# Performance work log

Hardware: AMD Instinct MI355X
Metric: run time of the kernel (lower is better)

## Reference

```python
import jax, jax.numpy as jnp
import numpy as np

N = 50000      # nodes
E = 800000     # edges
D_IN = 128     # irreps_in dim
SH = 16        # irreps_sh dim (lmax=3)
EA = 16        # edge_attr_dim
H = 8          # num_heads
DQ = 64        # irreps_query dim (8 per head)
DK = 64        # irreps_key dim (8 per head)
DV = 128       # irreps_out dim (16 per head)
HID = 64       # radial MLP hidden


def setup_inputs() -> dict:
    key = jax.random.key(0)
    ks = jax.random.split(key, 20)
    g = lambda k, shape, fan: jax.random.normal(k, shape, jnp.float32) / np.sqrt(fan)
    return {
        "node_attr": jax.random.normal(ks[0], (N, D_IN), jnp.float32),
        "edge_attr": jax.random.normal(ks[1], (E, EA), jnp.float32),
        "edge_sh": jax.random.normal(ks[2], (E, SH), jnp.float32),
        # h_q linear
        "Wq": g(ks[3], (D_IN, DQ), D_IN),
        # h_k conv: depthwise SH mixing, channel-mixing linear, radial MLP gate
        "Wang_k": g(ks[4], (D_IN, SH), SH),
        "Wlin_k": g(ks[5], (D_IN, DK), D_IN),
        "W1k": g(ks[6], (EA, HID), EA),
        "b1k": jnp.zeros((HID,), jnp.float32),
        "W2k": g(ks[7], (HID, DK), HID),
        # h_v conv
        "Wang_v": g(ks[8], (D_IN, SH), SH),
        "Wlin_v": g(ks[9], (D_IN, DV), D_IN),
        "W1v": g(ks[10], (EA, HID), EA),
        "b1v": jnp.zeros((HID,), jnp.float32),
        "W2v": g(ks[11], (HID, DV), HID),
        # FullyConnectedTensorProduct(query_per_head, key_per_head, '0e') -> weighted bilinear dot
        "Wdot": g(ks[12], (DQ // H, DK // H), DQ // H),
        # lin_out
        "Wout": g(ks[13], (DV, DV), DV),
        "edge_index": jax.random.randint(ks[14], (2, E), 0, N, jnp.int64),
    }


def _conv_per_edge(x_src, edge_attr, edge_sh, Wang, Wlin, W1, b1, W2):
    # depthwise tensor product of node feats with edge SH, channel mix, radial gate
    rad = jax.nn.relu(edge_attr @ W1 + b1) @ W2          # [E, Dout]
    g = edge_sh @ Wang.T                                  # [E, D_IN]
    return ((x_src * g) @ Wlin) * rad                     # [E, Dout]


def reference(node_attr, edge_attr, edge_sh, Wq, Wang_k, Wlin_k, W1k, b1k, W2k,
              Wang_v, Wlin_v, W1v, b1v, W2v, Wdot, Wout, edge_index):
    src, dst = edge_index[0], edge_index[1]
    n = node_attr.shape[0]
    e = src.shape[0]

    q = (node_attr @ Wq).reshape(n, H, DQ // H)           # [N,H,dq]
    x_src = node_attr[src]                                # gather [E,D_IN]
    k = _conv_per_edge(x_src, edge_attr, edge_sh, Wang_k, Wlin_k, W1k, b1k, W2k).reshape(e, H, DK // H)
    v = _conv_per_edge(x_src, edge_attr, edge_sh, Wang_v, Wlin_v, W1v, b1v, W2v).reshape(e, H, DV // H)

    # TP 'dot' to scalars: weighted bilinear per head
    alpha = jnp.einsum('ehq,qk,ehk->eh', q[dst], Wdot, k)  # [E,H]

    # scatter_softmax over incoming edges of each dst node
    amax = jax.ops.segment_max(alpha, dst, num_segments=n)  # [N,H]
    ealpha = jnp.exp(alpha - amax[dst])
    denom = jax.ops.segment_sum(ealpha, dst, num_segments=n)
    attn = ealpha / denom[dst]                              # [E,H]

    # weighted scatter-sum of values
    out = jax.ops.segment_sum(attn[..., None] * v, dst, num_segments=n)  # [N,H,dv]
    return out.reshape(n, DV) @ Wout
```

## Files before the change

### kernel.cpp

```cpp
#include <hip/hip_runtime.h>
#include <stdint.h>

#define NN 50000
#define NE 800000
#define STRIP 49

typedef unsigned int u32;
typedef uint16_t u16;

__device__ __forceinline__ float b2f(u16 u){ return __builtin_bit_cast(float, (u32)((u32)u << 16)); }
__device__ __forceinline__ float b2f_lo(u32 p){ return __builtin_bit_cast(float, p << 16); }
__device__ __forceinline__ float b2f_hi(u32 p){ return __builtin_bit_cast(float, p & 0xffff0000u); }
__device__ __forceinline__ u32 f2b_bits(float f){ u32 u = __builtin_bit_cast(u32, f); return (u + 0x7fffu + ((u >> 16) & 1u)) >> 16; }
__device__ __forceinline__ u16 f2b(float f){ return (u16)f2b_bits(f); }
__device__ __forceinline__ u32 packb(float lo, float hi){ return f2b_bits(lo) | (f2b_bits(hi) << 16); }

typedef __bf16 bf16x2 __attribute__((ext_vector_type(2)));
#if defined(__has_builtin)
#if __has_builtin(__builtin_amdgcn_fdot2_f32_bf16)
#define HAVE_DOT2_BUILTIN 1
#endif
#endif

#ifdef HAVE_DOT2_BUILTIN
__device__ __forceinline__ float dot2b(u32 a, u32 b, float c){
  return __builtin_amdgcn_fdot2_f32_bf16(__builtin_bit_cast(bf16x2, a),
                                         __builtin_bit_cast(bf16x2, b), c, false);
}
#else
__device__ __forceinline__ float dot2b(u32 a, u32 b, float c){
  c = fmaf(b2f_lo(a), b2f_lo(b), c);
  return fmaf(b2f_hi(a), b2f_hi(b), c);
}
#endif

typedef __attribute__((ext_vector_type(8))) short short8;
typedef __attribute__((ext_vector_type(4))) float f32x4;
__device__ __forceinline__ f32x4 mf32(uint4 a, uint4 b, f32x4 c){
  return __builtin_amdgcn_mfma_f32_16x16x32_bf16(
      __builtin_bit_cast(short8, a), __builtin_bit_cast(short8, b), c, 0, 0, 0);
}

#define OFF_WANG_V 0
#define OFF_W1_V   5120
#define OFF_WLIN_V 7680
#define OFF_W2_V   25088
#define OFF_WANG_K 34304
#define OFF_W1_K   39424
#define OFF_WLIN_K 41984
#define OFF_W2_K   50688
#define OFF_WOUT   55296
#define OFF_WQD    72704
#define WT_TOTAL   81408

__global__ __launch_bounds__(256) void zero_kernel(int* __restrict__ counts,
                                                   int* __restrict__ edge_ids)
{
  int i = blockIdx.x * 256 + threadIdx.x;
  if (i < NN) counts[i] = 0;
  if (i < NE) edge_ids[i] = 0;
}

__global__ __launch_bounds__(256) void prep_w_kernel(
    const float* __restrict__ Wang_v, const float* __restrict__ W1_v,
    const float* __restrict__ Wlin_v, const float* __restrict__ W2_v,
    const float* __restrict__ Wang_k, const float* __restrict__ W1_k,
    const float* __restrict__ Wlin_k, const float* __restrict__ W2_k,
    const float* __restrict__ Wout, const float* __restrict__ Wq,
    const float* __restrict__ Wdot,
    u16* __restrict__ wt)
{
  int idx = blockIdx.x * 256 + threadIdx.x;
  if (idx >= WT_TOTAL) return;
  float val = 0.f;
  if (idx < OFF_W1_V) {
    int l = idx - OFF_WANG_V, n = l / 40, k = l % 40;
    if (k >= 16 && k < 32) val = Wang_v[n * 16 + (k - 16)];
  } else if (idx < OFF_WLIN_V) {
    int l = idx - OFF_W1_V, n = l / 40, k = l % 40;
    if (k < 16) val = W1_v[k * 64 + n];
  } else if (idx < OFF_W2_V) {
    int l = idx - OFF_WLIN_V, n = l / 136, k = l % 136;
    if (k < 128) val = Wlin_v[k * 128 + n];
  } else if (idx < OFF_WANG_K) {
    int l = idx - OFF_W2_V, n = l / 72, k = l % 72;
    if (k < 64) val = W2_v[k * 128 + n];
  } else if (idx < OFF_W1_K) {
    int l = idx - OFF_WANG_K, n = l / 40, k = l % 40;
    if (k >= 16 && k < 32) val = Wang_k[n * 16 + (k - 16)];
  } else if (idx < OFF_WLIN_K) {
    int l = idx - OFF_W1_K, n = l / 40, k = l % 40;
    if (k < 16) val = W1_k[k * 64 + n];
  } else if (idx < OFF_W2_K) {
    int l = idx - OFF_WLIN_K, n = l / 136, k = l % 136;
    if (k < 128) val = Wlin_k[k * 64 + n];
  } else if (idx < OFF_WOUT) {
    int l = idx - OFF_W2_K, n = l / 72, k = l % 72;
    if (k < 64) val = W2_k[k * 64 + n];
  } else if (idx < OFF_WQD) {
    int l = idx - OFF_WOUT, n = l / 136, k = l % 136;
    if (k < 128) val = Wout[k * 128 + n];
  } else {
    int l = idx - OFF_WQD, n = l / 136, k = l % 136;
    if (k < 128) {
      int h = n >> 3, r = n & 7;
      float s = 0.f;
#pragma unroll
      for (int i = 0; i < 8; ++i) s += Wq[k * 64 + h * 8 + i] * Wdot[i * 8 + r];
      val = s;
    }
  }
  wt[idx] = f2b(val);
}

__global__ __launch_bounds__(256) void qw_kernel(const float* __restrict__ node_attr,
                                                 const u16* __restrict__ wt,
                                                 u16* __restrict__ qw)
{
  __shared__ __align__(16) u16 sX[64 * 136];
  uint4* sX4 = (uint4*)sX;
  u32* sX32 = (u32*)sX;
  const uint4* wt4 = (const uint4*)wt;
  const int tid = threadIdx.x, wv = tid >> 6, lane = tid & 63, lq = lane >> 4, ln = lane & 15;
  const int n0 = blockIdx.x * 64;
  uint4 rB[4];
#pragma unroll
  for (int ks = 0; ks < 4; ++ks) rB[ks] = wt4[9088 + (wv * 16 + ln) * 17 + ks * 4 + lq];
  {
    int row = tid >> 2, q4 = tid & 3;
    int n = n0 + row;
    bool valid = n < NN;
    const float4* xp = (const float4*)(node_attr + (size_t)(valid ? n : 0) * 128);
#pragma unroll
    for (int i = 0; i < 8; ++i) {
      float4 v = valid ? xp[q4 * 8 + i] : make_float4(0.f, 0.f, 0.f, 0.f);
      sX32[row * 68 + (q4 * 8 + i) * 2]     = packb(v.x, v.y);
      sX32[row * 68 + (q4 * 8 + i) * 2 + 1] = packb(v.z, v.w);
    }
  }
  __syncthreads();
  const f32x4 z4 = {0.f, 0.f, 0.f, 0.f};
  int col = wv * 16 + ln;
#pragma unroll
  for (int et = 0; et < 4; ++et) {
    f32x4 acc = z4;
#pragma unroll
    for (int ks = 0; ks < 4; ++ks) acc = mf32(sX4[(et * 16 + ln) * 17 + ks * 4 + lq], rB[ks], acc);
#pragma unroll
    for (int r = 0; r < 4; ++r) {
      int rr = n0 + et * 16 + lq * 4 + r;
      if (rr < NN) qw[(size_t)rr * 64 + col] = f2b(acc[r]);
    }
  }
}

__global__ __launch_bounds__(256, 2) void conv_fused_kernel(
    const float* __restrict__ node_attr, const float* __restrict__ edge_attr,
    const float* __restrict__ edge_sh, const int* __restrict__ edge_index,
    const float* __restrict__ b1v, const float* __restrict__ b1k,
    const u16* __restrict__ wt, const u16* __restrict__ qw,
    u16* __restrict__ v_out, float* __restrict__ alpha)
{
  __shared__ __align__(16) u16 sC[64 * 40];
  __shared__ __align__(16) u16 sX[64 * 136];
  __shared__ __align__(16) u16 sTk[64 * 136];
  __shared__ __align__(16) u16 sHv[64 * 72];
  __shared__ __align__(16) u16 sHk[64 * 72];
  uint4* sC4 = (uint4*)sC; u32* sC32 = (u32*)sC;
  uint4* sX4 = (uint4*)sX; u32* sX32 = (u32*)sX;
  uint4* sTk4 = (uint4*)sTk;
  uint4* sHv4 = (uint4*)sHv;
  uint4* sHk4 = (uint4*)sHk;
  const uint4* wt4 = (const uint4*)wt;

  const int tid = threadIdx.x;
  const int wv = tid >> 6, lane = tid & 63, lq = lane >> 4, ln = lane & 15;
  const int e0 = blockIdx.x * 64;
  const int nA = wv * 16 + ln, nB = (wv + 4) * 16 + ln;
  const int cb = wv * 16 + 4 * lq;

  const int el = tid >> 2, p = tid & 3;
  int dq = edge_index[NE + e0 + el]; if ((u32)dq >= NN) dq = 0;
  const uint4* qptr = (const uint4*)(qw + (size_t)dq * 64 + p * 16);
  uint4 q0 = qptr[0], q1 = qptr[1];

  uint4 rW1V    = wt4[640 + nA * 5 + lq];
  uint4 rW1K    = wt4[4928 + nA * 5 + lq];
  uint4 rWangV0 = wt4[nA * 5 + lq],        rWangV1 = wt4[nB * 5 + lq];
  uint4 rWangK0 = wt4[4288 + nA * 5 + lq], rWangK1 = wt4[4288 + nB * 5 + lq];
  uint4 rWlinV[2][4], rWlinK[4], rW2V[2][2], rW2K[2];
#pragma unroll
  for (int ks = 0; ks < 4; ++ks) {
    rWlinV[0][ks] = wt4[960 + nA * 17 + ks * 4 + lq];
    rWlinV[1][ks] = wt4[960 + nB * 17 + ks * 4 + lq];
    rWlinK[ks]    = wt4[5248 + nA * 17 + ks * 4 + lq];
  }
#pragma unroll
  for (int ks = 0; ks < 2; ++ks) {
    rW2V[0][ks] = wt4[3136 + nA * 9 + ks * 4 + lq];
    rW2V[1][ks] = wt4[3136 + nB * 9 + ks * 4 + lq];
    rW2K[ks]    = wt4[6336 + nA * 9 + ks * 4 + lq];
  }
  float4 bV = *(const float4*)(b1v + cb);
  float4 bK = *(const float4*)(b1k + cb);

  {
    int r = tid >> 2, kq = tid & 3;
    float4 ea = ((const float4*)(edge_attr + (size_t)(e0 + r) * 16))[kq];
    *(uint2*)(sC32 + r * 20 + kq * 2) = make_uint2(packb(ea.x, ea.y), packb(ea.z, ea.w));
    float4 sh = ((const float4*)(edge_sh + (size_t)(e0 + r) * 16))[kq];
    *(uint2*)(sC32 + r * 20 + 8 + kq * 2) = make_uint2(packb(sh.x, sh.y), packb(sh.z, sh.w));
  }
  {
    int g = tid >> 3, j = tid & 7;
#pragma unroll
    for (int rr = 0; rr < 2; ++rr) {
      int row = g + rr * 32;
      int s = edge_index[e0 + row]; if ((u32)s >= NN) s = 0;
      const float4* xp = (const float4*)(node_attr + (size_t)s * 128);
#pragma unroll
      for (int c = 0; c < 4; ++c) {
        float4 v = xp[c * 8 + j];
        *(uint2*)(sX32 + row * 68 + c * 16 + j * 2) =
            make_uint2(packb(v.x, v.y), packb(v.z, v.w));
      }
    }
  }
  __syncthreads();

  const f32x4 z4 = {0.f, 0.f, 0.f, 0.f};
#pragma unroll
  for (int et = 0; et < 4; ++et) {
    uint4 aC = sC4[(et * 16 + ln) * 5 + lq];
    f32x4 hv  = mf32(rW1V, aC, z4);
    f32x4 hk  = mf32(rW1K, aC, z4);
    f32x4 t0v = mf32(rWangV0, aC, z4);
    f32x4 t1v = mf32(rWangV1, aC, z4);
    f32x4 t0k = mf32(rWangK0, aC, z4);
    f32x4 t1k = mf32(rWangK1, aC, z4);
    const int edge = et * 16 + ln;
    u16* xr = sX + edge * 136 + cb;
    uint2 xa = *(const uint2*)xr;
    uint2 xb = *(const uint2*)(xr + 64);
    float x0 = b2f_lo(xa.x), x1 = b2f_hi(xa.x), x2 = b2f_lo(xa.y), x3 = b2f_hi(xa.y);
    float y0 = b2f_lo(xb.x), y1 = b2f_hi(xb.x), y2 = b2f_lo(xb.y), y3 = b2f_hi(xb.y);
    *(uint2*)xr = make_uint2(packb(t0v[0] * x0, t0v[1] * x1),
                             packb(t0v[2] * x2, t0v[3] * x3));
    *(uint2*)(xr + 64) = make_uint2(packb(t1v[0] * y0, t1v[1] * y1),
                                    packb(t1v[2] * y2, t1v[3] * y3));
    u16* tkr = sTk + edge * 136 + cb;
    *(uint2*)tkr = make_uint2(packb(t0k[0] * x0, t0k[1] * x1),
                              packb(t0k[2] * x2, t0k[3] * x3));
    *(uint2*)(tkr + 64) = make_uint2(packb(t1k[0] * y0, t1k[1] * y1),
                                     packb(t1k[2] * y2, t1k[3] * y3));
    *(uint2*)(sHv + edge * 72 + cb) = make_uint2(
        packb(fmaxf(hv[0] + bV.x, 0.f), fmaxf(hv[1] + bV.y, 0.f)),
        packb(fmaxf(hv[2] + bV.z, 0.f), fmaxf(hv[3] + bV.w, 0.f)));
    *(uint2*)(sHk + edge * 72 + cb) = make_uint2(
        packb(fmaxf(hk[0] + bK.x, 0.f), fmaxf(hk[1] + bK.y, 0.f)),
        packb(fmaxf(hk[2] + bK.z, 0.f), fmaxf(hk[3] + bK.w, 0.f)));
  }
  __syncthreads();

  f32x4 a1v0[4], a1v1[4], a1k[4], a2v0[4], a2v1[4], a2k[4];
#pragma unroll
  for (int et = 0; et < 4; ++et) {
    const int er = et * 16 + ln;
    f32x4 acc0 = z4, acc1 = z4, acck = z4;
#pragma unroll
    for (int ks = 0; ks < 4; ++ks) {
      uint4 tb = sX4[er * 17 + ks * 4 + lq];
      acc0 = mf32(rWlinV[0][ks], tb, acc0);
      acc1 = mf32(rWlinV[1][ks], tb, acc1);
      acck = mf32(rWlinK[ks], sTk4[er * 17 + ks * 4 + lq], acck);
    }
    a1v0[et] = acc0; a1v1[et] = acc1; a1k[et] = acck;
    f32x4 b0 = z4, b1 = z4, bk = z4;
#pragma unroll
    for (int ks = 0; ks < 2; ++ks) {
      uint4 hb = sHv4[er * 9 + ks * 4 + lq];
      b0 = mf32(rW2V[0][ks], hb, b0);
      b1 = mf32(rW2V[1][ks], hb, b1);
      bk = mf32(rW2K[ks], sHk4[er * 9 + ks * 4 + lq], bk);
    }
    a2v0[et] = b0; a2v1[et] = b1; a2k[et] = bk;
  }
  __syncthreads();

#pragma unroll
  for (int et = 0; et < 4; ++et) {
    const int edge = et * 16 + ln;
    u16* vr = sX + edge * 136 + cb;
    *(uint2*)vr = make_uint2(
        packb(a1v0[et][0] * a2v0[et][0], a1v0[et][1] * a2v0[et][1]),
        packb(a1v0[et][2] * a2v0[et][2], a1v0[et][3] * a2v0[et][3]));
    *(uint2*)(vr + 64) = make_uint2(
        packb(a1v1[et][0] * a2v1[et][0], a1v1[et][1] * a2v1[et][1]),
        packb(a1v1[et][2] * a2v1[et][2], a1v1[et][3] * a2v1[et][3]));
    *(uint2*)(sHk + edge * 72 + cb) = make_uint2(
        packb(a1k[et][0] * a2k[et][0], a1k[et][1] * a2k[et][1]),
        packb(a1k[et][2] * a2k[et][2], a1k[et][3] * a2k[et][3]));
  }
  __syncthreads();

  {
    int row = tid >> 2, seg = tid & 3;
    uint4* gp = (uint4*)(v_out + (size_t)(e0 + row) * 128);
#pragma unroll
    for (int i = 0; i < 4; ++i) gp[seg * 4 + i] = sX4[row * 17 + seg * 4 + i];
  }
  {
    uint4 k0 = sHk4[el * 9 + p * 2];
    uint4 k1 = sHk4[el * 9 + p * 2 + 1];
    float a0 = 0.f, a1 = 0.f;
    a0 = dot2b(q0.x, k0.x, a0); a0 = dot2b(q0.y, k0.y, a0);
    a0 = dot2b(q0.z, k0.z, a0); a0 = dot2b(q0.w, k0.w, a0);
    a1 = dot2b(q1.x, k1.x, a1); a1 = dot2b(q1.y, k1.y, a1);
    a1 = dot2b(q1.z, k1.z, a1); a1 = dot2b(q1.w, k1.w, a1);
    ((float2*)(alpha + (size_t)(e0 + el) * 8))[p] = make_float2(a0, a1);
  }
}

__global__ __launch_bounds__(256) void count_kernel(const int* __restrict__ edge_index,
                                                    int* __restrict__ counts)
{
  int e = blockIdx.x * 256 + threadIdx.x;
  if (e < NE) { int d = edge_index[NE + e]; if ((u32)d >= NN) d = 0; atomicAdd(&counts[d], 1); }
}

__global__ __launch_bounds__(1024) void scan_kernel(const int* __restrict__ counts,
                                                    int* __restrict__ row_ptr,
                                                    int* __restrict__ cursor)
{
  __shared__ int s[1024];
  int tid = threadIdx.x;
  int base = tid * STRIP;
  int sum = 0;
  for (int i = 0; i < STRIP; ++i) { int idx = base + i; sum += (idx < NN) ? counts[idx] : 0; }
  s[tid] = sum;
  __syncthreads();
  for (int off = 1; off < 1024; off <<= 1) {
    int v = s[tid];
    int add = (tid >= off) ? s[tid - off] : 0;
    __syncthreads();
    s[tid] = v + add;
    __syncthreads();
  }
  int running = (tid == 0) ? 0 : s[tid - 1];
  for (int i = 0; i < STRIP; ++i) {
    int idx = base + i;
    if (idx < NN) { row_ptr[idx] = running; cursor[idx] = running; running += counts[idx]; }
  }
  if (tid == 1023) row_ptr[NN] = running;
}

__global__ __launch_bounds__(256) void fill_kernel(const int* __restrict__ edge_index,
                                                   int* __restrict__ cursor,
                                                   int* __restrict__ edge_ids)
{
  int e = blockIdx.x * 256 + threadIdx.x;
  if (e < NE) {
    int dst = edge_index[NE + e]; if ((u32)dst >= NN) dst = 0;
    int pos = atomicAdd(&cursor[dst], 1);
    if ((u32)pos < NE) edge_ids[pos] = e;
  }
}

#define OUPD(aa, ww)                                                   \
  { float mn = fmaxf(m, (aa));                                         \
    float sc = __expf(m - mn);                                         \
    float pw = __expf((aa) - mn);                                      \
    l = l * sc + pw;                                                   \
    accA = accA * sc + pw * b2f_lo(ww);                                \
    accB = accB * sc + pw * b2f_hi(ww);                                \
    m = mn; }

__global__ __launch_bounds__(256) void out_kernel(
    const int* __restrict__ row_ptr, const int* __restrict__ edge_ids,
    const float* __restrict__ alpha, const u16* __restrict__ v_e,
    const u16* __restrict__ wt, float* __restrict__ out)
{
  __shared__ __align__(16) u16 sAgg[16 * 136];
  u32* sAgg32 = (u32*)sAgg;
  uint4* sAgg4 = (uint4*)sAgg;
  const uint4* wt4 = (const uint4*)wt;
  const u32* v32 = (const u32*)v_e;
  const int tid = threadIdx.x, wv = tid >> 6, lane = tid & 63, lq = lane >> 4, ln = lane & 15;
  const f32x4 z4 = {0.f, 0.f, 0.f, 0.f};
  uint4 rWT[2][4];
#pragma unroll
  for (int c = 0; c < 2; ++c) {
    int n = (wv * 2 + c) * 16 + ln;
#pragma unroll
    for (int ks = 0; ks < 4; ++ks) rWT[c][ks] = wt4[6912 + n * 17 + ks * 4 + lq];
  }
  const int hh = lane >> 3;
  const int grp = blockIdx.x;
#pragma unroll 1
  for (int i = 0; i < 4; ++i) {
    int n = grp * 16 + wv * 4 + i;
    int beg = row_ptr[n], end = row_ptr[n + 1];
    if (beg < 0) beg = 0; if (beg > NE) beg = NE;
    if (end < beg) end = beg; if (end > NE) end = NE;
    int deg = end - beg;
    float m = -3.0e38f, l = 0.f, accA = 0.f, accB = 0.f;
    int j = 0;
#pragma unroll 1
    for (; j + 4 <= deg; j += 4) {
      int e0 = edge_ids[beg + j],     e1 = edge_ids[beg + j + 1];
      int e2 = edge_ids[beg + j + 2], e3 = edge_ids[beg + j + 3];
      if ((u32)e0 >= NE) e0 = 0; if ((u32)e1 >= NE) e1 = 0;
      if ((u32)e2 >= NE) e2 = 0; if ((u32)e3 >= NE) e3 = 0;
      float a0 = alpha[(size_t)e0 * 8 + hh]; u32 w0 = v32[(size_t)e0 * 64 + lane];
      float a1 = alpha[(size_t)e1 * 8 + hh]; u32 w1 = v32[(size_t)e1 * 64 + lane];
      float a2 = alpha[(size_t)e2 * 8 + hh]; u32 w2 = v32[(size_t)e2 * 64 + lane];
      float a3 = alpha[(size_t)e3 * 8 + hh]; u32 w3 = v32[(size_t)e3 * 64 + lane];
      OUPD(a0, w0); OUPD(a1, w1); OUPD(a2, w2); OUPD(a3, w3);
    }
#pragma unroll 1
    for (; j < deg; ++j) {
      int e = edge_ids[beg + j]; if ((u32)e >= NE) e = 0;
      float a = alpha[(size_t)e * 8 + hh]; u32 w = v32[(size_t)e * 64 + lane];
      OUPD(a, w);
    }
    float inv = (l > 0.f) ? (1.f / l) : 0.f;
    accA *= inv; accB *= inv;
    sAgg32[(wv * 4 + i) * 68 + lane] = packb(accA, accB);
  }
  __syncthreads();
#pragma unroll
  for (int c = 0; c < 2; ++c) {
    f32x4 acc = z4;
#pragma unroll
    for (int ks = 0; ks < 4; ++ks) acc = mf32(sAgg4[ln * 17 + ks * 4 + lq], rWT[c][ks], acc);
    int col = (wv * 2 + c) * 16 + ln;
#pragma unroll
    for (int r = 0; r < 4; ++r)
      out[(size_t)(grp * 16 + lq * 4 + r) * 128 + col] = acc[r];
  }
}

extern "C" void kernel_launch(void* const* d_in, const int* in_sizes, int n_in,
                              void* d_out, int out_size, void* d_ws, size_t ws_size,
                              hipStream_t stream)
{
  const float* node_attr = (const float*)d_in[0];
  const float* edge_attr = (const float*)d_in[1];
  const float* edge_sh   = (const float*)d_in[2];
  const float* Wq        = (const float*)d_in[3];
  const float* Wang_k    = (const float*)d_in[4];
  const float* Wlin_k    = (const float*)d_in[5];
  const float* W1k       = (const float*)d_in[6];
  const float* b1k       = (const float*)d_in[7];
  const float* W2k       = (const float*)d_in[8];
  const float* Wang_v    = (const float*)d_in[9];
  const float* Wlin_v    = (const float*)d_in[10];
  const float* W1v       = (const float*)d_in[11];
  const float* b1v       = (const float*)d_in[12];
  const float* W2v       = (const float*)d_in[13];
  const float* Wdot      = (const float*)d_in[14];
  const float* Wout      = (const float*)d_in[15];
  const int* edge_index  = (const int*)d_in[16];
  float* out = (float*)d_out;

  char* ws = (char*)d_ws;
  u16*   v_e      = (u16*)(ws + 0);
  float* alpha    = (float*)(ws + 204800000);
  u16*   qw       = (u16*)(ws + 230400000);
  int*   counts   = (int*)(ws + 236800000);
  int*   row_ptr  = (int*)(ws + 237000064);
  int*   cursor   = (int*)(ws + 237200128);
  int*   edge_ids = (int*)(ws + 237400192);
  u16*   wt       = (u16*)(ws + 240600192);

  zero_kernel<<<dim3((NE + 255) / 256), dim3(256), 0, stream>>>(counts, edge_ids);
  prep_w_kernel<<<dim3((WT_TOTAL + 255) / 256), dim3(256), 0, stream>>>(
      Wang_v, W1v, Wlin_v, W2v, Wang_k, W1k, Wlin_k, W2k, Wout, Wq, Wdot, wt);
  qw_kernel<<<dim3((NN + 63) / 64), dim3(256), 0, stream>>>(node_attr, wt, qw);
  conv_fused_kernel<<<dim3(NE / 64), dim3(256), 0, stream>>>(
      node_attr, edge_attr, edge_sh, edge_index, b1v, b1k, wt, qw, v_e, alpha);
  count_kernel<<<dim3((NE + 255) / 256), dim3(256), 0, stream>>>(edge_index, counts);
  scan_kernel<<<dim3(1), dim3(1024), 0, stream>>>(counts, row_ptr, cursor);
  fill_kernel<<<dim3((NE + 255) / 256), dim3(256), 0, stream>>>(edge_index, cursor, edge_ids);
  out_kernel<<<dim3(3125), dim3(256), 0, stream>>>(row_ptr, edge_ids, alpha, v_e, wt, out);
}
```

Baseline: 673.5 us.

## Permute channel layout, gather node features directly into registers, use hardware bf16 pack

```diff
diff --git a/kernel.cpp b/kernel.cpp
--- a/kernel.cpp
+++ b/kernel.cpp
@@ -13,7 +13,11 @@
 __device__ __forceinline__ float b2f_hi(u32 p){ return __builtin_bit_cast(float, p & 0xffff0000u); }
 __device__ __forceinline__ u32 f2b_bits(float f){ u32 u = __builtin_bit_cast(u32, f); return (u + 0x7fffu + ((u >> 16) & 1u)) >> 16; }
 __device__ __forceinline__ u16 f2b(float f){ return (u16)f2b_bits(f); }
-__device__ __forceinline__ u32 packb(float lo, float hi){ return f2b_bits(lo) | (f2b_bits(hi) << 16); }
+__device__ __forceinline__ u32 packb(float lo, float hi){
+  u32 r;
+  asm("v_cvt_pk_bf16_f32 %0, %1, %2" : "=v"(r) : "v"(lo), "v"(hi));
+  return r;
+}
 
 typedef __bf16 bf16x2 __attribute__((ext_vector_type(2)));
 #if defined(__has_builtin)
@@ -39,6 +43,10 @@
 __device__ __forceinline__ f32x4 mf32(uint4 a, uint4 b, f32x4 c){
   return __builtin_amdgcn_mfma_f32_16x16x32_bf16(
       __builtin_bit_cast(short8, a), __builtin_bit_cast(short8, b), c, 0, 0, 0);
+}
+
+__device__ __forceinline__ int chperm(int n){
+  return 32 * ((n & 63) >> 4) + 8 * ((n & 15) >> 2) + 4 * (n >> 6) + (n & 3);
 }
 
 #define OFF_WANG_V 0
@@ -75,19 +83,19 @@
   float val = 0.f;
   if (idx < OFF_W1_V) {
     int l = idx - OFF_WANG_V, n = l / 40, k = l % 40;
-    if (k >= 16 && k < 32) val = Wang_v[n * 16 + (k - 16)];
+    if (k >= 16 && k < 32) val = Wang_v[chperm(n) * 16 + (k - 16)];
   } else if (idx < OFF_WLIN_V) {
     int l = idx - OFF_W1_V, n = l / 40, k = l % 40;
     if (k < 16) val = W1_v[k * 64 + n];
   } else if (idx < OFF_W2_V) {
     int l = idx - OFF_WLIN_V, n = l / 136, k = l % 136;
-    if (k < 128) val = Wlin_v[k * 128 + n];
+    if (k < 128) val = Wlin_v[k * 128 + chperm(n)];
   } else if (idx < OFF_WANG_K) {
     int l = idx - OFF_W2_V, n = l / 72, k = l % 72;
-    if (k < 64) val = W2_v[k * 128 + n];
+    if (k < 64) val = W2_v[k * 128 + chperm(n)];
   } else if (idx < OFF_W1_K) {
     int l = idx - OFF_WANG_K, n = l / 40, k = l % 40;
-    if (k >= 16 && k < 32) val = Wang_k[n * 16 + (k - 16)];
+    if (k >= 16 && k < 32) val = Wang_k[chperm(n) * 16 + (k - 16)];
   } else if (idx < OFF_WLIN_K) {
     int l = idx - OFF_W1_K, n = l / 40, k = l % 40;
     if (k < 16) val = W1_k[k * 64 + n];
@@ -167,7 +175,7 @@
   __shared__ __align__(16) u16 sHv[64 * 72];
   __shared__ __align__(16) u16 sHk[64 * 72];
   uint4* sC4 = (uint4*)sC; u32* sC32 = (u32*)sC;
-  uint4* sX4 = (uint4*)sX; u32* sX32 = (u32*)sX;
+  uint4* sX4 = (uint4*)sX;
   uint4* sTk4 = (uint4*)sTk;
   uint4* sHv4 = (uint4*)sHv;
   uint4* sHk4 = (uint4*)sHk;
@@ -177,30 +185,26 @@
   const int wv = tid >> 6, lane = tid & 63, lq = lane >> 4, ln = lane & 15;
   const int e0 = blockIdx.x * 64;
   const int nA = wv * 16 + ln, nB = (wv + 4) * 16 + ln;
-  const int cb = wv * 16 + 4 * lq;
+  const int cb  = wv * 16 + 4 * lq;
+  const int cb8 = wv * 32 + 8 * lq;
 
   const int el = tid >> 2, p = tid & 3;
   int dq = edge_index[NE + e0 + el]; if ((u32)dq >= NN) dq = 0;
   const uint4* qptr = (const uint4*)(qw + (size_t)dq * 64 + p * 16);
   uint4 q0 = qptr[0], q1 = qptr[1];
 
+  int srcs[4];
+#pragma unroll
+  for (int et = 0; et < 4; ++et) {
+    int s = edge_index[e0 + et * 16 + ln];
+    if ((u32)s >= NN) s = 0;
+    srcs[et] = s;
+  }
+
   uint4 rW1V    = wt4[640 + nA * 5 + lq];
   uint4 rW1K    = wt4[4928 + nA * 5 + lq];
   uint4 rWangV0 = wt4[nA * 5 + lq],        rWangV1 = wt4[nB * 5 + lq];
   uint4 rWangK0 = wt4[4288 + nA * 5 + lq], rWangK1 = wt4[4288 + nB * 5 + lq];
-  uint4 rWlinV[2][4], rWlinK[4], rW2V[2][2], rW2K[2];
-#pragma unroll
-  for (int ks = 0; ks < 4; ++ks) {
-    rWlinV[0][ks] = wt4[960 + nA * 17 + ks * 4 + lq];
-    rWlinV[1][ks] = wt4[960 + nB * 17 + ks * 4 + lq];
-    rWlinK[ks]    = wt4[5248 + nA * 17 + ks * 4 + lq];
-  }
-#pragma unroll
-  for (int ks = 0; ks < 2; ++ks) {
-    rW2V[0][ks] = wt4[3136 + nA * 9 + ks * 4 + lq];
-    rW2V[1][ks] = wt4[3136 + nB * 9 + ks * 4 + lq];
-    rW2K[ks]    = wt4[6336 + nA * 9 + ks * 4 + lq];
-  }
   float4 bV = *(const float4*)(b1v + cb);
   float4 bK = *(const float4*)(b1k + cb);
 
@@ -211,26 +215,20 @@
     float4 sh = ((const float4*)(edge_sh + (size_t)(e0 + r) * 16))[kq];
     *(uint2*)(sC32 + r * 20 + 8 + kq * 2) = make_uint2(packb(sh.x, sh.y), packb(sh.z, sh.w));
   }
-  {
-    int g = tid >> 3, j = tid & 7;
-#pragma unroll
-    for (int rr = 0; rr < 2; ++rr) {
-      int row = g + rr * 32;
-      int s = edge_index[e0 + row]; if ((u32)s >= NN) s = 0;
-      const float4* xp = (const float4*)(node_attr + (size_t)s * 128);
-#pragma unroll
-      for (int c = 0; c < 4; ++c) {
-        float4 v = xp[c * 8 + j];
-        *(uint2*)(sX32 + row * 68 + c * 16 + j * 2) =
-            make_uint2(packb(v.x, v.y), packb(v.z, v.w));
-      }
-    }
-  }
+  const float* xp0 = node_attr + (size_t)srcs[0] * 128 + cb8;
+  float4 xa = *(const float4*)xp0;
+  float4 xb = *(const float4*)(xp0 + 4);
   __syncthreads();
 
   const f32x4 z4 = {0.f, 0.f, 0.f, 0.f};
 #pragma unroll
   for (int et = 0; et < 4; ++et) {
+    float4 xa_n, xb_n;
+    if (et < 3) {
+      const float* xp = node_attr + (size_t)srcs[et + 1] * 128 + cb8;
+      xa_n = *(const float4*)xp;
+      xb_n = *(const float4*)(xp + 4);
+    }
     uint4 aC = sC4[(et * 16 + ln) * 5 + lq];
     f32x4 hv  = mf32(rW1V, aC, z4);
     f32x4 hk  = mf32(rW1K, aC, z4);
@@ -239,30 +237,37 @@
     f32x4 t0k = mf32(rWangK0, aC, z4);
     f32x4 t1k = mf32(rWangK1, aC, z4);
     const int edge = et * 16 + ln;
-    u16* xr = sX + edge * 136 + cb;
-    uint2 xa = *(const uint2*)xr;
-    uint2 xb = *(const uint2*)(xr + 64);
-    float x0 = b2f_lo(xa.x), x1 = b2f_hi(xa.x), x2 = b2f_lo(xa.y), x3 = b2f_hi(xa.y);
-    float y0 = b2f_lo(xb.x), y1 = b2f_hi(xb.x), y2 = b2f_lo(xb.y), y3 = b2f_hi(xb.y);
-    *(uint2*)xr = make_uint2(packb(t0v[0] * x0, t0v[1] * x1),
-                             packb(t0v[2] * x2, t0v[3] * x3));
-    *(uint2*)(xr + 64) = make_uint2(packb(t1v[0] * y0, t1v[1] * y1),
-                                    packb(t1v[2] * y2, t1v[3] * y3));
-    u16* tkr = sTk + edge * 136 + cb;
-    *(uint2*)tkr = make_uint2(packb(t0k[0] * x0, t0k[1] * x1),
-                              packb(t0k[2] * x2, t0k[3] * x3));
-    *(uint2*)(tkr + 64) = make_uint2(packb(t1k[0] * y0, t1k[1] * y1),
-                                     packb(t1k[2] * y2, t1k[3] * y3));
+    sX4[edge * 17 + 4 * wv + lq] = make_uint4(
+        packb(t0v[0] * xa.x, t0v[1] * xa.y), packb(t0v[2] * xa.z, t0v[3] * xa.w),
+        packb(t1v[0] * xb.x, t1v[1] * xb.y), packb(t1v[2] * xb.z, t1v[3] * xb.w));
+    sTk4[edge * 17 + 4 * wv + lq] = make_uint4(
+        packb(t0k[0] * xa.x, t0k[1] * xa.y), packb(t0k[2] * xa.z, t0k[3] * xa.w),
+        packb(t1k[0] * xb.x, t1k[1] * xb.y), packb(t1k[2] * xb.z, t1k[3] * xb.w));
     *(uint2*)(sHv + edge * 72 + cb) = make_uint2(
         packb(fmaxf(hv[0] + bV.x, 0.f), fmaxf(hv[1] + bV.y, 0.f)),
         packb(fmaxf(hv[2] + bV.z, 0.f), fmaxf(hv[3] + bV.w, 0.f)));
     *(uint2*)(sHk + edge * 72 + cb) = make_uint2(
         packb(fmaxf(hk[0] + bK.x, 0.f), fmaxf(hk[1] + bK.y, 0.f)),
         packb(fmaxf(hk[2] + bK.z, 0.f), fmaxf(hk[3] + bK.w, 0.f)));
-  }
-  __syncthreads();
-
-  f32x4 a1v0[4], a1v1[4], a1k[4], a2v0[4], a2v1[4], a2k[4];
+    xa = xa_n; xb = xb_n;
+  }
+
+  uint4 rWlinV[2][4], rWlinK[4], rW2V[2][2], rW2K[2];
+#pragma unroll
+  for (int ks = 0; ks < 4; ++ks) {
+    rWlinV[0][ks] = wt4[960 + nA * 17 + ks * 4 + lq];
+    rWlinV[1][ks] = wt4[960 + nB * 17 + ks * 4 + lq];
+    rWlinK[ks]    = wt4[5248 + nA * 17 + ks * 4 + lq];
+  }
+#pragma unroll
+  for (int ks = 0; ks < 2; ++ks) {
+    rW2V[0][ks] = wt4[3136 + nA * 9 + ks * 4 + lq];
+    rW2V[1][ks] = wt4[3136 + nB * 9 + ks * 4 + lq];
+    rW2K[ks]    = wt4[6336 + nA * 9 + ks * 4 + lq];
+  }
+  __syncthreads();
+
+  uint4 pv[4]; uint2 pk[4];
 #pragma unroll
   for (int et = 0; et < 4; ++et) {
     const int er = et * 16 + ln;
@@ -274,7 +279,6 @@
       acc1 = mf32(rWlinV[1][ks], tb, acc1);
       acck = mf32(rWlinK[ks], sTk4[er * 17 + ks * 4 + lq], acck);
     }
-    a1v0[et] = acc0; a1v1[et] = acc1; a1k[et] = acck;
     f32x4 b0 = z4, b1 = z4, bk = z4;
 #pragma unroll
     for (int ks = 0; ks < 2; ++ks) {
@@ -283,23 +287,20 @@
       b1 = mf32(rW2V[1][ks], hb, b1);
       bk = mf32(rW2K[ks], sHk4[er * 9 + ks * 4 + lq], bk);
     }
-    a2v0[et] = b0; a2v1[et] = b1; a2k[et] = bk;
+    pv[et] = make_uint4(packb(acc0[0] * b0[0], acc0[1] * b0[1]),
+                        packb(acc0[2] * b0[2], acc0[3] * b0[3]),
+                        packb(acc1[0] * b1[0], acc1[1] * b1[1]),
+                        packb(acc1[2] * b1[2], acc1[3] * b1[3]));
+    pk[et] = make_uint2(packb(acck[0] * bk[0], acck[1] * bk[1]),
+                        packb(acck[2] * bk[2], acck[3] * bk[3]));
   }
   __syncthreads();
 
 #pragma unroll
   for (int et = 0; et < 4; ++et) {
     const int edge = et * 16 + ln;
-    u16* vr = sX + edge * 136 + cb;
-    *(uint2*)vr = make_uint2(
-        packb(a1v0[et][0] * a2v0[et][0], a1v0[et][1] * a2v0[et][1]),
-        packb(a1v0[et][2] * a2v0[et][2], a1v0[et][3] * a2v0[et][3]));
-    *(uint2*)(vr + 64) = make_uint2(
-        packb(a1v1[et][0] * a2v1[et][0], a1v1[et][1] * a2v1[et][1]),
-        packb(a1v1[et][2] * a2v1[et][2], a1v1[et][3] * a2v1[et][3]));
-    *(uint2*)(sHk + edge * 72 + cb) = make_uint2(
-        packb(a1k[et][0] * a2k[et][0], a1k[et][1] * a2k[et][1]),
-        packb(a1k[et][2] * a2k[et][2], a1k[et][3] * a2k[et][3]));
+    sX4[edge * 17 + 4 * wv + lq] = pv[et];
+    *(uint2*)(sHk + edge * 72 + cb) = pk[et];
   }
   __syncthreads();
 
```

New measurement: 680.9 us. About the same (+1.1%).
